# Optimization experiments

Hardware: AMD Instinct MI355X
Metric: run time of the kernel (lower is better)

The kernel has to match this reference:

```python
import jax, jax.numpy as jnp
import numpy as np

N = 100000        # nodes
E = 1600000       # edges (before self-loops)
F_IN = 128        # input feature dim
HID = 32          # hidden_channels
HEADS = 2
HC = HID * HEADS  # 64, per-conv output width (concat=True)
OUT = 40          # out_channels
NEG_SLOPE = 0.2   # PyG GATConv leaky_relu slope
BN_EPS = 1e-5


def setup_inputs() -> dict:
    key = jax.random.key(0)
    ks = jax.random.split(key, 16)
    g = lambda k, shape, s: jax.random.normal(k, shape, jnp.float32) * s
    node_feat = jax.random.normal(ks[0], (N, F_IN), jnp.float32)
    edge_index = jax.random.randint(ks[1], (2, E), 0, N, jnp.int32)
    inp = {
        "node_feat": node_feat,
        "edge_index": edge_index,
        "W1": g(ks[2], (F_IN, HC), 1.0 / np.sqrt(F_IN)),
        "a_src1": g(ks[3], (HEADS, HID), 0.1),
        "a_dst1": g(ks[4], (HEADS, HID), 0.1),
        "b1": jnp.zeros((HC,), jnp.float32),
        # BatchNorm1d(64) in eval mode (running stats)
        "bn_gamma": jnp.ones((HC,), jnp.float32),
        "bn_beta": jnp.zeros((HC,), jnp.float32),
        "bn_mean": g(ks[5], (HC,), 0.1),
        "bn_var": jax.random.uniform(ks[6], (HC,), jnp.float32, 0.5, 1.5),
        "W2": g(ks[7], (HC, HC), 1.0 / np.sqrt(HC)),
        "a_src2": g(ks[8], (HEADS, HID), 0.1),
        "a_dst2": g(ks[9], (HEADS, HID), 0.1),
        "b2": jnp.zeros((HC,), jnp.float32),
        # final projection 64 -> 40
        "Wf": g(ks[10], (HC, OUT), 1.0 / np.sqrt(HC)),
        "bf": jnp.zeros((OUT,), jnp.float32),
    }
    return inp


def _gat_layer(x, src, dst, W, a_s, a_d, b):
    # x: [N, Fin] -> h: [N, H, C]
    h = (x @ W).reshape(N, HEADS, HID)
    alpha_src = jnp.einsum('nhc,hc->nh', h, a_s)   # [N, H]
    alpha_dst = jnp.einsum('nhc,hc->nh', h, a_d)   # [N, H]
    e = jax.nn.leaky_relu(alpha_src[src] + alpha_dst[dst], NEG_SLOPE)  # [Etot, H]
    m = jax.lax.stop_gradient(jax.ops.segment_max(e, dst, num_segments=N))
    ex = jnp.exp(e - m[dst])
    denom = jax.ops.segment_sum(ex, dst, num_segments=N)
    alpha = ex / (denom[dst] + 1e-16)              # softmax over incoming edges
    msg = h[src] * alpha[:, :, None]               # [Etot, H, C]
    out = jax.ops.segment_sum(msg, dst, num_segments=N)  # [N, H, C]
    return out.reshape(N, HC) + b


def reference(node_feat, edge_index, W1, a_src1, a_dst1, b1,
              bn_gamma, bn_beta, bn_mean, bn_var,
              W2, a_src2, a_dst2, b2, Wf, bf):
    # add self-loops (PyG GATConv default add_self_loops=True)
    loop = jnp.arange(N, dtype=edge_index.dtype)
    src = jnp.concatenate([edge_index[0], loop])
    dst = jnp.concatenate([edge_index[1], loop])

    x1 = _gat_layer(node_feat, src, dst, W1, a_src1, a_dst1, b1)
    # BatchNorm1d eval + ELU (dropout is identity in eval)
    x1 = (x1 - bn_mean) * (bn_gamma / jnp.sqrt(bn_var + BN_EPS)) + bn_beta
    x1 = jax.nn.elu(x1)

    x2 = _gat_layer(x1, src, dst, W2, a_src2, a_dst2, b2)

    # JumpingKnowledge 'max': elementwise max over layer outputs
    xj = jnp.maximum(x1, x2)
    return xj @ Wf + bf
```

## Files before the change

### kernel.cpp

```cpp
#include <hip/hip_runtime.h>
#include <hip/hip_bf16.h>

#define N_NODES 100000
#define E_EDGES 1600000
#define ETOT    1700000
#define EQ8     200000
#define NB_EQ8  782
#define NGB     1563
#define NBUK    196
#define F_IN    128
#define HC      64
#define OUT_C   40
#define NEG_SLOPE 0.2f
#define BN_EPS  1e-5f

#define P_W1   0
#define P_AS1  8192
#define P_AD1  8256
#define P_B1   8320
#define P_BNG  8384
#define P_BNB  8448
#define P_BNM  8512
#define P_BNV  8576
#define P_W2   8640
#define P_AS2  12736
#define P_AD2  12800
#define P_B2   12864
#define P_WF   12928
#define P_BF   15488
#define P_TOT  15528

typedef __attribute__((ext_vector_type(8))) short short8;
typedef __attribute__((ext_vector_type(4))) float floatx4;
typedef __attribute__((ext_vector_type(4))) unsigned int uintx4;

__device__ __forceinline__ unsigned short f2bf(float f) {
    unsigned int u = __float_as_uint(f);
    unsigned int r = u + 0x7FFFu + ((u >> 16) & 1u);
    return (unsigned short)(r >> 16);
}

__device__ __forceinline__ float leaky(float v) { return v > 0.f ? v : NEG_SLOPE * v; }

__device__ __forceinline__ float red64(float v) {
#pragma unroll
    for (int off = 32; off > 0; off >>= 1) v += __shfl_xor(v, off, 64);
    return v;
}
__device__ __forceinline__ float red16(float v) {
#pragma unroll
    for (int off = 8; off > 0; off >>= 1) v += __shfl_xor(v, off, 64);
    return v;
}

__global__ __launch_bounds__(64) void detect_kernel(const unsigned short* __restrict__ x,
                                                    int* __restrict__ flag) {
    int t = threadIdx.x;
    bool huge = false;
#pragma unroll
    for (int i = 0; i < 4; ++i) {
        unsigned short u = x[(t * 4 + i) * 2];
        float v = __uint_as_float(((unsigned int)u) << 16);
        if (!(fabsf(v) < 1e4f)) huge = true;
    }
    unsigned long long b = __ballot(huge);
    if (t == 0) *flag = (b != 0ull) ? 1 : 0;
}

struct CvtArgs { const void* ptr[14]; int len[14]; };

__global__ __launch_bounds__(256) void cvt_params_kernel(CvtArgs a,
                                                         const int* __restrict__ flag,
                                                         float* __restrict__ dst) {
    int f = *flag;
    int i = blockIdx.x * 256 + threadIdx.x;
    if (i >= P_TOT) return;
    int k = 0, off = 0;
    while (i >= off + a.len[k]) { off += a.len[k]; ++k; }
    int j = i - off;
    float v = f ? ((const float*)a.ptr[k])[j]
                : __bfloat162float(((const __hip_bfloat16*)a.ptr[k])[j]);
    dst[i] = v;
}

__global__ __launch_bounds__(256) void build_frags_kernel(const float* __restrict__ prm,
                                                          unsigned short* __restrict__ fw1,
                                                          unsigned short* __restrict__ fw2) {
    int i = blockIdx.x * 256 + threadIdx.x;
    if (i < 8192) {
        int j = i & 7, l = (i >> 3) & 63, q = (i >> 9) & 3, t = i >> 11;
        int k = q * 32 + (l >> 4) * 8 + j;
        int n = t * 16 + (l & 15);
        fw1[i] = f2bf(prm[P_W1 + k * 64 + n]);
    } else if (i < 12288) {
        int f = i - 8192;
        int j = f & 7, l = (f >> 3) & 63, q = (f >> 9) & 1, t = f >> 10;
        int k = q * 32 + (l >> 4) * 8 + j;
        int n = t * 16 + (l & 15);
        fw2[f] = f2bf(prm[P_W2 + k * 64 + n]);
    }
}


__global__ __launch_bounds__(256) void fused_hist_gemm1_kernel(
        const int* __restrict__ ei, int* __restrict__ bkt_cnt,
        const void* __restrict__ x, const unsigned short* __restrict__ fw1,
        const float* __restrict__ prm, const int* __restrict__ flag,
        unsigned short* __restrict__ h_bf, float* __restrict__ as_,
        float* __restrict__ ad_) {
    __shared__ short lx[4 * 4 * 64 * 8];
    int t = threadIdx.x;
    if (blockIdx.x < NB_EQ8) {
        int* cnt = (int*)lx;
        if (t < NBUK) cnt[t] = 0;
        __syncthreads();
        int i8 = blockIdx.x * 256 + t;
        if (i8 < EQ8) {
            const unsigned long long* dst2 = (const unsigned long long*)(ei + E_EDGES);
            unsigned long long p0 = __builtin_nontemporal_load(&dst2[i8 * 4]);
            unsigned long long p1 = __builtin_nontemporal_load(&dst2[i8 * 4 + 1]);
            unsigned long long p2 = __builtin_nontemporal_load(&dst2[i8 * 4 + 2]);
            unsigned long long p3 = __builtin_nontemporal_load(&dst2[i8 * 4 + 3]);
            atomicAdd(&cnt[(int)(p0 & 0xFFFFFFFFull) >> 9], 1);
            atomicAdd(&cnt[(int)(p0 >> 32) >> 9], 1);
            atomicAdd(&cnt[(int)(p1 & 0xFFFFFFFFull) >> 9], 1);
            atomicAdd(&cnt[(int)(p1 >> 32) >> 9], 1);
            atomicAdd(&cnt[(int)(p2 & 0xFFFFFFFFull) >> 9], 1);
            atomicAdd(&cnt[(int)(p2 >> 32) >> 9], 1);
            atomicAdd(&cnt[(int)(p3 & 0xFFFFFFFFull) >> 9], 1);
            atomicAdd(&cnt[(int)(p3 >> 32) >> 9], 1);
        }
        __syncthreads();
        if (t < NBUK) {
            int tb = t + (int)(blockIdx.x % NBUK);
            tb -= (tb >= NBUK) ? NBUK : 0;
            int c = cnt[tb];
            if (c) atomicAdd(&bkt_cnt[tb], c);
        }
        return;
    }

    int f = *flag;
    int base = (blockIdx.x - NB_EQ8) * 64;

#pragma unroll
    for (int i = 0; i < 4; ++i) {
        int cid = i * 256 + t;
        int m = cid >> 4, c = cid & 15;
        int q = c >> 2, g = c & 3;
        int loff = (((m >> 4) * 4 + q) * 64 + g * 16 + (m & 15)) * 8;
        int srow = base + m; if (srow > N_NODES - 1) srow = N_NODES - 1;
        short8 s;
        if (f) {
            const float4* p = (const float4*)((const float*)x + ((size_t)srow << 7) + (c << 3));
            float4 u0 = p[0], u1 = p[1];
            s[0] = (short)f2bf(u0.x); s[1] = (short)f2bf(u0.y);
            s[2] = (short)f2bf(u0.z); s[3] = (short)f2bf(u0.w);
            s[4] = (short)f2bf(u1.x); s[5] = (short)f2bf(u1.y);
            s[6] = (short)f2bf(u1.z); s[7] = (short)f2bf(u1.w);
        } else {
            s = *(const short8*)((const unsigned short*)x + ((size_t)srow << 7) + (c << 3));
        }
        *(short8*)&lx[loff] = s;
    }
    __syncthreads();

    int w = t >> 6, lane = t & 63;
    short8 a[4];
#pragma unroll
    for (int q = 0; q < 4; ++q) a[q] = *(short8*)&lx[((w * 4 + q) * 64 + lane) * 8];

    const short8* bw = (const short8*)fw1;
    floatx4 acc[4];
#pragma unroll
    for (int tt = 0; tt < 4; ++tt) acc[tt] = (floatx4){0.f, 0.f, 0.f, 0.f};
#pragma unroll
    for (int tt = 0; tt < 4; ++tt) {
#pragma unroll
        for (int q = 0; q < 4; ++q) {
            short8 b = bw[(tt * 4 + q) * 64 + lane];
            acc[tt] = __builtin_amdgcn_mfma_f32_16x16x32_bf16(a[q], b, acc[tt], 0, 0, 0);
        }
    }

    int cl = lane & 15, grp = lane >> 4;
#pragma unroll
    for (int tt = 0; tt < 4; ++tt) {
#pragma unroll
        for (int r = 0; r < 4; ++r) {
            int node = base + w * 16 + grp * 4 + r;
            if (node < N_NODES)
                h_bf[(size_t)node * 64 + tt * 16 + cl] = f2bf(acc[tt][r]);
        }
    }

    float as0 = prm[P_AS1 + 0  + cl], as1 = prm[P_AS1 + 16 + cl],
          as2 = prm[P_AS1 + 32 + cl], as3 = prm[P_AS1 + 48 + cl];
    float ad0 = prm[P_AD1 + 0  + cl], ad1 = prm[P_AD1 + 16 + cl],
          ad2 = prm[P_AD1 + 32 + cl], ad3 = prm[P_AD1 + 48 + cl];
#pragma unroll
    for (int r = 0; r < 4; ++r) {
        float sh0 = red16(acc[0][r] * as0 + acc[1][r] * as1);
        float sh1 = red16(acc[2][r] * as2 + acc[3][r] * as3);
        float dh0 = red16(acc[0][r] * ad0 + acc[1][r] * ad1);
        float dh1 = red16(acc[2][r] * ad2 + acc[3][r] * ad3);
        int node = base + w * 16 + grp * 4 + r;
        if (cl == 0 && node < N_NODES) {
            as_[node * 2] = sh0;  as_[node * 2 + 1] = sh1;
            ad_[node * 2] = dh0;  ad_[node * 2 + 1] = dh1;
        }
    }
}

__global__ __launch_bounds__(256) void bucket_scan_kernel(const int* __restrict__ bkt_cnt,
                                                          int* __restrict__ boff,
                                                          int* __restrict__ bcur,
                                                          int* __restrict__ row_start) {
    __shared__ int sm[256];
    int t = threadIdx.x;
    int v = (t < NBUK) ? bkt_cnt[t] : 0;
    sm[t] = v;
    __syncthreads();
    for (int off = 1; off < 256; off <<= 1) {
        int o = (t >= off) ? sm[t - off] : 0;
        __syncthreads();
        sm[t] += o;
        __syncthreads();
    }
    if (t < NBUK) { int e = sm[t] - v; boff[t] = e; bcur[t] = e; }
    if (t == NBUK - 1) boff[NBUK] = sm[t];
    if (t == 0) row_start[N_NODES] = ETOT;
}

__global__ __launch_bounds__(256) void bucket_scatter_kernel(const int* __restrict__ ei,
                                                             int* __restrict__ bcur,
                                                             unsigned long long* __restrict__ estage) {
    __shared__ int cnt[NBUK];
    __shared__ int base[NBUK];
    int t = threadIdx.x;
    if (t < NBUK) cnt[t] = 0;
    __syncthreads();
    int i8 = blockIdx.x * 256 + t;
    bool valid = i8 < EQ8;
    int d[8], s[8], rl[8];
    if (valid) {
        const unsigned long long* dst2 = (const unsigned long long*)(ei + E_EDGES);
        const unsigned long long* src2 = (const unsigned long long*)ei;
        unsigned long long p0 = __builtin_nontemporal_load(&dst2[i8 * 4]);
        unsigned long long p1 = __builtin_nontemporal_load(&dst2[i8 * 4 + 1]);
        unsigned long long p2 = __builtin_nontemporal_load(&dst2[i8 * 4 + 2]);
        unsigned long long p3 = __builtin_nontemporal_load(&dst2[i8 * 4 + 3]);
        unsigned long long q0 = __builtin_nontemporal_load(&src2[i8 * 4]);
        unsigned long long q1 = __builtin_nontemporal_load(&src2[i8 * 4 + 1]);
        unsigned long long q2 = __builtin_nontemporal_load(&src2[i8 * 4 + 2]);
        unsigned long long q3 = __builtin_nontemporal_load(&src2[i8 * 4 + 3]);
        d[0] = (int)(p0 & 0xFFFFFFFFull); d[1] = (int)(p0 >> 32);
        d[2] = (int)(p1 & 0xFFFFFFFFull); d[3] = (int)(p1 >> 32);
        d[4] = (int)(p2 & 0xFFFFFFFFull); d[5] = (int)(p2 >> 32);
        d[6] = (int)(p3 & 0xFFFFFFFFull); d[7] = (int)(p3 >> 32);
        s[0] = (int)(q0 & 0xFFFFFFFFull); s[1] = (int)(q0 >> 32);
        s[2] = (int)(q1 & 0xFFFFFFFFull); s[3] = (int)(q1 >> 32);
        s[4] = (int)(q2 & 0xFFFFFFFFull); s[5] = (int)(q2 >> 32);
        s[6] = (int)(q3 & 0xFFFFFFFFull); s[7] = (int)(q3 >> 32);
#pragma unroll
        for (int k = 0; k < 8; ++k) rl[k] = atomicAdd(&cnt[d[k] >> 9], 1);
    }
    __syncthreads();
    if (t < NBUK) {
        int tb = t + (int)(blockIdx.x % NBUK);
        tb -= (tb >= NBUK) ? NBUK : 0;
        int c = cnt[tb];
        base[tb] = c ? atomicAdd(&bcur[tb], c) : 0;
    }
    __syncthreads();
    if (valid) {
#pragma unroll
        for (int k = 0; k < 8; ++k) {
            int buk = d[k] >> 9;
            estage[base[buk] + rl[k]] =
                (unsigned long long)(unsigned int)s[k] |
                ((unsigned long long)(unsigned int)d[k] << 32);
        }
    }
}

__global__ __launch_bounds__(256) void bucket_csr_kernel(const unsigned long long* __restrict__ estage,
                                                         const int* __restrict__ boff,
                                                         int* __restrict__ row_start,
                                                         int* __restrict__ col) {
    __shared__ int ldeg[512];
    __shared__ int sA[512], sB[512];
    __shared__ int exq[512];
    int b = blockIdx.x, t = threadIdx.x;
    int nbase = b << 9;
    int nb = N_NODES - nbase; if (nb > 512) nb = 512;
    int e0 = boff[b], e1 = boff[b + 1];
    int rb = e0 + nbase;
    ldeg[t] = 0; ldeg[t + 256] = 0;
    __syncthreads();
    for (int e = e0 + t; e < e1; e += 256) {
        int dl = (int)(estage[e] >> 32) - nbase;
        atomicAdd(&ldeg[dl], 1);
    }
    __syncthreads();
    int v0 = (t < nb) ? ldeg[t] + 1 : 0;
    int v1 = (t + 256 < nb) ? ldeg[t + 256] + 1 : 0;
    sA[t] = v0; sA[t + 256] = v1;
    __syncthreads();
    int* A = sA; int* Bp = sB;
    for (int off = 1; off < 512; off <<= 1) {
        int a0 = A[t] + ((t >= off) ? A[t - off] : 0);
        int a1 = A[t + 256] + ((t + 256 >= off) ? A[t + 256 - off] : 0);
        Bp[t] = a0; Bp[t + 256] = a1;
        __syncthreads();
        int* tmp = A; A = Bp; Bp = tmp;
    }
    exq[t] = A[t] - v0;
    exq[t + 256] = A[t + 256] - v1;
    __syncthreads();
    if (t < nb) { int rsv = rb + exq[t]; row_start[nbase + t] = rsv; col[rsv] = nbase + t; }
    if (t + 256 < nb) { int rsv = rb + exq[t + 256]; row_start[nbase + t + 256] = rsv; col[rsv] = nbase + t + 256; }
    ldeg[t] = 0; ldeg[t + 256] = 0;
    __syncthreads();
    for (int e = e0 + t; e < e1; e += 256) {
        unsigned long long p = estage[e];
        int s = (int)(p & 0xFFFFFFFFull);
        int dl = (int)(p >> 32) - nbase;
        int r = atomicAdd(&ldeg[dl], 1);
        col[rb + exq[dl] + 1 + r] = s;
    }
}

__global__ __launch_bounds__(128) void gemm2_kernel(const unsigned short* __restrict__ x1_bf,
                                                    const unsigned short* __restrict__ fw2,
                                                    const float* __restrict__ prm,
                                                    unsigned short* __restrict__ h_bf,
                                                    float* __restrict__ as_,
                                                    float* __restrict__ ad_) {
    __shared__ short lx[2 * 2 * 64 * 8];
    int t = threadIdx.x;
    int base = blockIdx.x * 32;

#pragma unroll
    for (int i = 0; i < 2; ++i) {
        int cid = i * 128 + t;
        int m = cid >> 3, c = cid & 7;
        int q = c >> 2, g = c & 3;
        int loff = (((m >> 4) * 2 + q) * 64 + g * 16 + (m & 15)) * 8;
        short8 s = *(const short8*)(x1_bf + ((size_t)(base + m) << 6) + (c << 3));
        *(short8*)&lx[loff] = s;
    }
    __syncthreads();

    int w = t >> 6, lane = t & 63;
    short8 a[2];
#pragma unroll
    for (int q = 0; q < 2; ++q) a[q] = *(short8*)&lx[((w * 2 + q) * 64 + lane) * 8];

    const short8* bw = (const short8*)fw2;
    floatx4 acc[4];
#pragma unroll
    for (int tt = 0; tt < 4; ++tt) acc[tt] = (floatx4){0.f, 0.f, 0.f, 0.f};
#pragma unroll
    for (int tt = 0; tt < 4; ++tt) {
#pragma unroll
        for (int q = 0; q < 2; ++q) {
            short8 b = bw[(tt * 2 + q) * 64 + lane];
            acc[tt] = __builtin_amdgcn_mfma_f32_16x16x32_bf16(a[q], b, acc[tt], 0, 0, 0);
        }
    }

    int cl = lane & 15, grp = lane >> 4;
#pragma unroll
    for (int tt = 0; tt < 4; ++tt) {
#pragma unroll
        for (int r = 0; r < 4; ++r) {
            int node = base + w * 16 + grp * 4 + r;
            h_bf[(size_t)node * 64 + tt * 16 + cl] = f2bf(acc[tt][r]);
        }
    }

    float as0 = prm[P_AS2 + 0  + cl], as1 = prm[P_AS2 + 16 + cl],
          as2 = prm[P_AS2 + 32 + cl], as3 = prm[P_AS2 + 48 + cl];
    float ad0 = prm[P_AD2 + 0  + cl], ad1 = prm[P_AD2 + 16 + cl],
          ad2 = prm[P_AD2 + 32 + cl], ad3 = prm[P_AD2 + 48 + cl];
#pragma unroll
    for (int r = 0; r < 4; ++r) {
        float sh0 = red16(acc[0][r] * as0 + acc[1][r] * as1);
        float sh1 = red16(acc[2][r] * as2 + acc[3][r] * as3);
        float dh0 = red16(acc[0][r] * ad0 + acc[1][r] * ad1);
        float dh1 = red16(acc[2][r] * ad2 + acc[3][r] * ad3);
        if (cl == 0) {
            int node = base + w * 16 + grp * 4 + r;
            as_[node * 2] = sh0;  as_[node * 2 + 1] = sh1;
            ad_[node * 2] = dh0;  ad_[node * 2 + 1] = dh1;
        }
    }
}

__device__ __forceinline__ float slot_reduce(float acc[8], int lane) {
    int slot = lane & 7;
    bool b2 = (slot & 4) != 0;
#pragma unroll
    for (int q = 0; q < 4; ++q) {
        float send = b2 ? acc[q] : acc[q + 4];
        float recv = __shfl_xor(send, 4, 64);
        acc[q] = (b2 ? acc[q + 4] : acc[q]) + recv;
    }
    bool b1 = (slot & 2) != 0;
#pragma unroll
    for (int q = 0; q < 2; ++q) {
        float send = b1 ? acc[q] : acc[q + 2];
        float recv = __shfl_xor(send, 2, 64);
        acc[q] = (b1 ? acc[q + 2] : acc[q]) + recv;
    }
    bool b0 = (slot & 1) != 0;
    float send = b0 ? acc[0] : acc[1];
    float recv = __shfl_xor(send, 1, 64);
    return (b0 ? acc[1] : acc[0]) + recv;
}

template<int NK>
__device__ __forceinline__ void agg_rounds(const unsigned short* __restrict__ hb,
                                           const float* __restrict__ as_,
                                           const int* __restrict__ col,
                                           int rs, int koff, int last,
                                           int slot, int hi, float advh,
                                           float acc[8], float& sw) {
    int ce[NK]; float av[NK]; uintx4 dv[NK];
#pragma unroll
    for (int k = 0; k < NK; ++k) {
        int e = rs + koff + k * 8 + slot;
        ce[k] = col[e < last ? e : last];
    }
#pragma unroll
    for (int k = 0; k < NK; ++k)
        dv[k] = *(const uintx4*)(hb + ((size_t)ce[k] << 6));
#pragma unroll
    for (int k = 0; k < NK; ++k)
        av[k] = as_[ce[k] * 2 + hi];

    if constexpr (NK == 1) {
        asm volatile("" : "+v"(dv[0]), "+v"(av[0]));
    } else if constexpr (NK == 2) {
        asm volatile("" : "+v"(dv[0]), "+v"(dv[1]), "+v"(av[0]), "+v"(av[1]));
    } else if constexpr (NK == 3) {
        asm volatile("" : "+v"(dv[0]), "+v"(dv[1]), "+v"(dv[2]),
                          "+v"(av[0]), "+v"(av[1]), "+v"(av[2]));
    } else {
        asm volatile("" : "+v"(dv[0]), "+v"(dv[1]), "+v"(dv[2]), "+v"(dv[3]),
                          "+v"(av[0]), "+v"(av[1]), "+v"(av[2]), "+v"(av[3]));
    }

#pragma unroll
    for (int k = 0; k < NK; ++k) {
        int e = rs + koff + k * 8 + slot;
        float w = (e <= last) ? __expf(leaky(av[k] + advh)) : 0.f;
        sw += w;
#pragma unroll
        for (int q = 0; q < 4; ++q) {
            unsigned int dw = dv[k][q];
            acc[2 * q]     = fmaf(w, __uint_as_float(dw << 16),         acc[2 * q]);
            acc[2 * q + 1] = fmaf(w, __uint_as_float(dw & 0xFFFF0000u), acc[2 * q + 1]);
        }
    }
}

__device__ __forceinline__ float agg_core(const unsigned short* __restrict__ h_bf,
                                          const float* __restrict__ as_,
                                          const float* __restrict__ ad_,
                                          const int* __restrict__ col,
                                          int v, int rs, int re, int lane) {
    int deg  = re - rs;
    int slot = lane & 7;
    int cg   = lane >> 3;
    int hi   = cg >> 2;
    if (deg <= 64) {
        float advh = ad_[v * 2 + hi];
        const unsigned short* hb = h_bf + (cg << 3);
        int last = re - 1;
        float acc[8] = {0.f,0.f,0.f,0.f,0.f,0.f,0.f,0.f};
        float sw = 0.f;

        if (deg <= 8) {
            agg_rounds<1>(hb, as_, col, rs, 0, last, slot, hi, advh, acc, sw);
        } else if (deg <= 16) {
            agg_rounds<2>(hb, as_, col, rs, 0, last, slot, hi, advh, acc, sw);
        } else if (deg <= 24) {
            agg_rounds<3>(hb, as_, col, rs, 0, last, slot, hi, advh, acc, sw);
        } else {
            agg_rounds<4>(hb, as_, col, rs, 0, last, slot, hi, advh, acc, sw);
            if (deg > 32)
                agg_rounds<4>(hb, as_, col, rs, 32, last, slot, hi, advh, acc, sw);
        }

        sw += __shfl_xor(sw, 1, 64);
        sw += __shfl_xor(sw, 2, 64);
        sw += __shfl_xor(sw, 4, 64);
        float rdh = 1.f / (sw + 1e-16f);

        return slot_reduce(acc, lane) * rdh;
    } else {
        int head = lane >> 5;
        float adv0 = ad_[v * 2], adv1 = ad_[v * 2 + 1];
        float advh = head ? adv1 : adv0;
        float s0 = 0.f, s1 = 0.f;
        for (int e = rs + lane; e < re; e += 64) {
            int s = col[e];
            float2 av = *(const float2*)&as_[s * 2];
            s0 += __expf(leaky(av.x + adv0));
            s1 += __expf(leaky(av.y + adv1));
        }
        s0 = red64(s0); s1 = red64(s1);
        float rdh = 1.f / ((head ? s1 : s0) + 1e-16f);
        float a0 = 0.f;
        for (int e = rs; e < re; ++e) {
            int s = col[e];
            float w = __expf(leaky(as_[s * 2 + head] + advh));
            unsigned short u = h_bf[(size_t)s * 64 + lane];
            a0 = fmaf(w, __uint_as_float(((unsigned int)u) << 16), a0);
        }
        return a0 * rdh;
    }
}

__global__ __launch_bounds__(256, 6) void agg1_kernel(const unsigned short* __restrict__ h_bf,
                                                   const float* __restrict__ as_,
                                                   const float* __restrict__ ad_,
                                                   const int* __restrict__ row_start,
                                                   const int* __restrict__ col,
                                                   const float* __restrict__ bias,
                                                   const float* __restrict__ bn_g,
                                                   const float* __restrict__ bn_b,
                                                   const float* __restrict__ bn_m,
                                                   const float* __restrict__ bn_v,
                                                   unsigned short* __restrict__ x1_bf) {
    int t = threadIdx.x, wid = t >> 6, lane = t & 63;
    int v = blockIdx.x * 4 + wid;
    int rs = row_start[v], re = row_start[v + 1];
    float acc = agg_core(h_bf, as_, ad_, col, v, rs, re, lane);
    float r = acc + bias[lane];
    float scale = bn_g[lane] * rsqrtf(bn_v[lane] + BN_EPS);
    r = (r - bn_m[lane]) * scale + bn_b[lane];
    r = r > 0.f ? r : expm1f(r);
    x1_bf[(size_t)v * 64 + lane] = f2bf(r);
}

__global__ __launch_bounds__(256, 6) void agg2_kernel(const unsigned short* __restrict__ h_bf,
                                                   const float* __restrict__ as_,
                                                   const float* __restrict__ ad_,
                                                   const int* __restrict__ row_start,
                                                   const int* __restrict__ col,
                                                   const float* __restrict__ prm,
                                                   const unsigned short* __restrict__ x1_bf,
                                                   const int* __restrict__ flag,
                                                   void* __restrict__ out) {
    __shared__ float Wfs[2560];
    __shared__ float xsh[4][64];
    int t = threadIdx.x;
#pragma unroll
    for (int i = 0; i < 10; ++i) Wfs[i * 256 + t] = prm[P_WF + i * 256 + t];

    int wid = t >> 6, lane = t & 63;
    int v = blockIdx.x * 4 + wid;
    int rs = row_start[v], re = row_start[v + 1];
    float acc = agg_core(h_bf, as_, ad_, col, v, rs, re, lane);
    float x2 = acc + prm[P_B2 + lane];
    unsigned short u = x1_bf[(size_t)v * 64 + lane];
    float x1v = __uint_as_float(((unsigned int)u) << 16);
    xsh[wid][lane] = fmaxf(x1v, x2);
    __syncthreads();

    if (t < 160) {
        int n = t / 40, o = t - n * 40;
        float po = 0.f;
#pragma unroll
        for (int c = 0; c < 64; c += 4) {
            po = fmaf(xsh[n][c],     Wfs[c * 40 + o],       po);
            po = fmaf(xsh[n][c + 1], Wfs[(c + 1) * 40 + o], po);
            po = fmaf(xsh[n][c + 2], Wfs[(c + 2) * 40 + o], po);
            po = fmaf(xsh[n][c + 3], Wfs[(c + 3) * 40 + o], po);
        }
        float r = po + prm[P_BF + o];
        size_t idx = (size_t)(blockIdx.x * 4 + n) * 40 + o;
        if (*flag) ((float*)out)[idx] = r;
        else ((__hip_bfloat16*)out)[idx] = __float2bfloat16(r);
    }
}

extern "C" void kernel_launch(void* const* d_in, const int* in_sizes, int n_in,
                              void* d_out, int out_size, void* d_ws, size_t ws_size,
                              hipStream_t stream) {
    (void)in_sizes; (void)n_in; (void)out_size; (void)ws_size;
    const void* node_feat = d_in[0];
    const int*  edge_idx  = (const int*)d_in[1];

    char* ws = (char*)d_ws;
    size_t off = 0;
    auto alloc = [&](size_t bytes) -> void* {
        void* p = ws + off;
        off += (bytes + 255) & ~(size_t)255;
        return p;
    };
    unsigned short* h_bf  = (unsigned short*)alloc((size_t)N_NODES * 64 * 2);
    unsigned short* x1_bf = (unsigned short*)alloc((size_t)N_NODES * 64 * 2);
    float* as_ = (float*)alloc((size_t)N_NODES * 2 * 4);
    float* ad_ = (float*)alloc((size_t)N_NODES * 2 * 4);
    int* row_start = (int*)alloc((size_t)(N_NODES + 1) * 4);
    unsigned long long* estage = (unsigned long long*)alloc((size_t)E_EDGES * 8);
    int* col       = (int*)alloc((size_t)ETOT * 4);
    int* bkt_cnt   = (int*)alloc((size_t)NBUK * 4);
    int* bkt_off   = (int*)alloc((size_t)(NBUK + 1) * 4);
    int* bkt_cur   = (int*)alloc((size_t)NBUK * 4);
    float* prm     = (float*)alloc((size_t)P_TOT * 4);
    unsigned short* fw1 = (unsigned short*)alloc(8192 * 2);
    unsigned short* fw2 = (unsigned short*)alloc(4096 * 2);
    int* flag      = (int*)alloc(256);

    detect_kernel<<<1, 64, 0, stream>>>((const unsigned short*)node_feat, flag);
    CvtArgs ca;
    const int lens[14] = {8192, 64, 64, 64, 64, 64, 64, 64, 4096, 64, 64, 64, 2560, 40};
    for (int i = 0; i < 14; ++i) { ca.ptr[i] = d_in[i + 2]; ca.len[i] = lens[i]; }
    cvt_params_kernel<<<(P_TOT + 255) / 256, 256, 0, stream>>>(ca, flag, prm);
    build_frags_kernel<<<48, 256, 0, stream>>>(prm, fw1, fw2);

    hipMemsetAsync(bkt_cnt, 0, (size_t)NBUK * 4, stream);
    fused_hist_gemm1_kernel<<<NB_EQ8 + NGB, 256, 0, stream>>>(
        edge_idx, bkt_cnt, node_feat, fw1, prm, flag, h_bf, as_, ad_);
    bucket_scan_kernel<<<1, 256, 0, stream>>>(bkt_cnt, bkt_off, bkt_cur, row_start);
    bucket_scatter_kernel<<<NB_EQ8, 256, 0, stream>>>(edge_idx, bkt_cur, estage);
    bucket_csr_kernel<<<NBUK, 256, 0, stream>>>(estage, bkt_off, row_start, col);

    agg1_kernel<<<N_NODES / 4, 256, 0, stream>>>(h_bf, as_, ad_, row_start, col,
                                                 prm + P_B1, prm + P_BNG, prm + P_BNB,
                                                 prm + P_BNM, prm + P_BNV, x1_bf);
    gemm2_kernel<<<N_NODES / 32, 128, 0, stream>>>(x1_bf, fw2, prm,
                                                   h_bf, as_, ad_);
    agg2_kernel<<<N_NODES / 4, 256, 0, stream>>>(h_bf, as_, ad_, row_start, col,
                                                 prm, x1_bf, flag, d_out);
}
```

Baseline: 333.7 us.

## Fuse layer-2 GEMM and attention logits into layer-1 aggregation kernel

Removes the separate MFMA gemm2 kernel. The layer-1 aggregation now stages W2 (16 KB fp32) in shared memory per block and computes each node's 64-wide h2 row with scalar FMAs, then reduces the attention source/destination logits across 32-lane halves. Separate h2/as2/ad2 buffers avoid overwriting layer-1 data still being read by other blocks. This saves a launch and the re-read of x1, but each 4-node block reloads W2 from global, uses 16 KB of LDS, and launch bounds rise to 8 waves per SIMD target, which may limit occupancy or cause spills.

Measured after the change: 338.4 us. Within noise of the previous version (+1.4%).

```diff
diff --git a/kernel.cpp b/kernel.cpp
--- a/kernel.cpp
+++ b/kernel.cpp
@@ -52,6 +52,11 @@
     for (int off = 8; off > 0; off >>= 1) v += __shfl_xor(v, off, 64);
     return v;
 }
+__device__ __forceinline__ float red32h(float v) {
+#pragma unroll
+    for (int off = 16; off > 0; off >>= 1) v += __shfl_xor(v, off, 64);
+    return v;
+}
 
 __global__ __launch_bounds__(64) void detect_kernel(const unsigned short* __restrict__ x,
                                                     int* __restrict__ flag) {
@@ -84,23 +89,15 @@
 }
 
 __global__ __launch_bounds__(256) void build_frags_kernel(const float* __restrict__ prm,
-                                                          unsigned short* __restrict__ fw1,
-                                                          unsigned short* __restrict__ fw2) {
+                                                          unsigned short* __restrict__ fw1) {
     int i = blockIdx.x * 256 + threadIdx.x;
     if (i < 8192) {
         int j = i & 7, l = (i >> 3) & 63, q = (i >> 9) & 3, t = i >> 11;
         int k = q * 32 + (l >> 4) * 8 + j;
         int n = t * 16 + (l & 15);
         fw1[i] = f2bf(prm[P_W1 + k * 64 + n]);
-    } else if (i < 12288) {
-        int f = i - 8192;
-        int j = f & 7, l = (f >> 3) & 63, q = (f >> 9) & 1, t = f >> 10;
-        int k = q * 32 + (l >> 4) * 8 + j;
-        int n = t * 16 + (l & 15);
-        fw2[f] = f2bf(prm[P_W2 + k * 64 + n]);
-    }
-}
-
+    }
+}
 
 __global__ __launch_bounds__(256) void fused_hist_gemm1_kernel(
         const int* __restrict__ ei, int* __restrict__ bkt_cnt,
@@ -331,73 +328,6 @@
     }
 }
 
-__global__ __launch_bounds__(128) void gemm2_kernel(const unsigned short* __restrict__ x1_bf,
-                                                    const unsigned short* __restrict__ fw2,
-                                                    const float* __restrict__ prm,
-                                                    unsigned short* __restrict__ h_bf,
-                                                    float* __restrict__ as_,
-                                                    float* __restrict__ ad_) {
-    __shared__ short lx[2 * 2 * 64 * 8];
-    int t = threadIdx.x;
-    int base = blockIdx.x * 32;
-
-#pragma unroll
-    for (int i = 0; i < 2; ++i) {
-        int cid = i * 128 + t;
-        int m = cid >> 3, c = cid & 7;
-        int q = c >> 2, g = c & 3;
-        int loff = (((m >> 4) * 2 + q) * 64 + g * 16 + (m & 15)) * 8;
-        short8 s = *(const short8*)(x1_bf + ((size_t)(base + m) << 6) + (c << 3));
-        *(short8*)&lx[loff] = s;
-    }
-    __syncthreads();
-
-    int w = t >> 6, lane = t & 63;
-    short8 a[2];
-#pragma unroll
-    for (int q = 0; q < 2; ++q) a[q] = *(short8*)&lx[((w * 2 + q) * 64 + lane) * 8];
-
-    const short8* bw = (const short8*)fw2;
-    floatx4 acc[4];
-#pragma unroll
-    for (int tt = 0; tt < 4; ++tt) acc[tt] = (floatx4){0.f, 0.f, 0.f, 0.f};
-#pragma unroll
-    for (int tt = 0; tt < 4; ++tt) {
-#pragma unroll
-        for (int q = 0; q < 2; ++q) {
-            short8 b = bw[(tt * 2 + q) * 64 + lane];
-            acc[tt] = __builtin_amdgcn_mfma_f32_16x16x32_bf16(a[q], b, acc[tt], 0, 0, 0);
-        }
-    }
-
-    int cl = lane & 15, grp = lane >> 4;
-#pragma unroll
-    for (int tt = 0; tt < 4; ++tt) {
-#pragma unroll
-        for (int r = 0; r < 4; ++r) {
-            int node = base + w * 16 + grp * 4 + r;
-            h_bf[(size_t)node * 64 + tt * 16 + cl] = f2bf(acc[tt][r]);
-        }
-    }
-
-    float as0 = prm[P_AS2 + 0  + cl], as1 = prm[P_AS2 + 16 + cl],
-          as2 = prm[P_AS2 + 32 + cl], as3 = prm[P_AS2 + 48 + cl];
-    float ad0 = prm[P_AD2 + 0  + cl], ad1 = prm[P_AD2 + 16 + cl],
-          ad2 = prm[P_AD2 + 32 + cl], ad3 = prm[P_AD2 + 48 + cl];
-#pragma unroll
-    for (int r = 0; r < 4; ++r) {
-        float sh0 = red16(acc[0][r] * as0 + acc[1][r] * as1);
-        float sh1 = red16(acc[2][r] * as2 + acc[3][r] * as3);
-        float dh0 = red16(acc[0][r] * ad0 + acc[1][r] * ad1);
-        float dh1 = red16(acc[2][r] * ad2 + acc[3][r] * ad3);
-        if (cl == 0) {
-            int node = base + w * 16 + grp * 4 + r;
-            as_[node * 2] = sh0;  as_[node * 2 + 1] = sh1;
-            ad_[node * 2] = dh0;  ad_[node * 2 + 1] = dh1;
-        }
-    }
-}
-
 __device__ __forceinline__ float slot_reduce(float acc[8], int lane) {
     int slot = lane & 7;
     bool b2 = (slot & 4) != 0;
@@ -524,31 +454,54 @@
     }
 }
 
-__global__ __launch_bounds__(256, 6) void agg1_kernel(const unsigned short* __restrict__ h_bf,
-                                                   const float* __restrict__ as_,
-                                                   const float* __restrict__ ad_,
-                                                   const int* __restrict__ row_start,
-                                                   const int* __restrict__ col,
-                                                   const float* __restrict__ bias,
-                                                   const float* __restrict__ bn_g,
-                                                   const float* __restrict__ bn_b,
-                                                   const float* __restrict__ bn_m,
-                                                   const float* __restrict__ bn_v,
-                                                   unsigned short* __restrict__ x1_bf) {
-    int t = threadIdx.x, wid = t >> 6, lane = t & 63;
+__global__ __launch_bounds__(256, 8) void agg1g2_kernel(
+        const unsigned short* __restrict__ h_bf,
+        const float* __restrict__ as_, const float* __restrict__ ad_,
+        const int* __restrict__ row_start, const int* __restrict__ col,
+        const float* __restrict__ prm,
+        unsigned short* __restrict__ x1_bf,
+        unsigned short* __restrict__ h2_bf,
+        float* __restrict__ as2_, float* __restrict__ ad2_) {
+    __shared__ float Wsh[4096];
+    __shared__ float xsh[4][64];
+    int t = threadIdx.x;
+#pragma unroll
+    for (int i = 0; i < 16; ++i) Wsh[i * 256 + t] = prm[P_W2 + i * 256 + t];
+
+    int wid = t >> 6, lane = t & 63;
     int v = blockIdx.x * 4 + wid;
     int rs = row_start[v], re = row_start[v + 1];
     float acc = agg_core(h_bf, as_, ad_, col, v, rs, re, lane);
-    float r = acc + bias[lane];
-    float scale = bn_g[lane] * rsqrtf(bn_v[lane] + BN_EPS);
-    r = (r - bn_m[lane]) * scale + bn_b[lane];
+    float r = acc + prm[P_B1 + lane];
+    float scale = prm[P_BNG + lane] * rsqrtf(prm[P_BNV + lane] + BN_EPS);
+    r = (r - prm[P_BNM + lane]) * scale + prm[P_BNB + lane];
     r = r > 0.f ? r : expm1f(r);
     x1_bf[(size_t)v * 64 + lane] = f2bf(r);
-}
-
-__global__ __launch_bounds__(256, 6) void agg2_kernel(const unsigned short* __restrict__ h_bf,
-                                                   const float* __restrict__ as_,
-                                                   const float* __restrict__ ad_,
+    xsh[wid][lane] = r;
+    __syncthreads();
+
+    float h2 = 0.f;
+#pragma unroll
+    for (int c = 0; c < 64; c += 4) {
+        h2 = fmaf(xsh[wid][c],     Wsh[c * 64 + lane],       h2);
+        h2 = fmaf(xsh[wid][c + 1], Wsh[(c + 1) * 64 + lane], h2);
+        h2 = fmaf(xsh[wid][c + 2], Wsh[(c + 2) * 64 + lane], h2);
+        h2 = fmaf(xsh[wid][c + 3], Wsh[(c + 3) * 64 + lane], h2);
+    }
+    h2_bf[(size_t)v * 64 + lane] = f2bf(h2);
+
+    float sh = red32h(h2 * prm[P_AS2 + lane]);
+    float dh = red32h(h2 * prm[P_AD2 + lane]);
+    if ((lane & 31) == 0) {
+        int hh = lane >> 5;
+        as2_[v * 2 + hh] = sh;
+        ad2_[v * 2 + hh] = dh;
+    }
+}
+
+__global__ __launch_bounds__(256, 8) void agg2_kernel(const unsigned short* __restrict__ h2_bf,
+                                                   const float* __restrict__ as2_,
+                                                   const float* __restrict__ ad2_,
                                                    const int* __restrict__ row_start,
                                                    const int* __restrict__ col,
                                                    const float* __restrict__ prm,
@@ -564,7 +517,7 @@
     int wid = t >> 6, lane = t & 63;
     int v = blockIdx.x * 4 + wid;
     int rs = row_start[v], re = row_start[v + 1];
-    float acc = agg_core(h_bf, as_, ad_, col, v, rs, re, lane);
+    float acc = agg_core(h2_bf, as2_, ad2_, col, v, rs, re, lane);
     float x2 = acc + prm[P_B2 + lane];
     unsigned short u = x1_bf[(size_t)v * 64 + lane];
     float x1v = __uint_as_float(((unsigned int)u) << 16);
@@ -603,9 +556,12 @@
         return p;
     };
     unsigned short* h_bf  = (unsigned short*)alloc((size_t)N_NODES * 64 * 2);
+    unsigned short* h2_bf = (unsigned short*)alloc((size_t)N_NODES * 64 * 2);
     unsigned short* x1_bf = (unsigned short*)alloc((size_t)N_NODES * 64 * 2);
-    float* as_ = (float*)alloc((size_t)N_NODES * 2 * 4);
-    float* ad_ = (float*)alloc((size_t)N_NODES * 2 * 4);
+    float* as_  = (float*)alloc((size_t)N_NODES * 2 * 4);
+    float* ad_  = (float*)alloc((size_t)N_NODES * 2 * 4);
+    float* as2_ = (float*)alloc((size_t)N_NODES * 2 * 4);
+    float* ad2_ = (float*)alloc((size_t)N_NODES * 2 * 4);
     int* row_start = (int*)alloc((size_t)(N_NODES + 1) * 4);
     unsigned long long* estage = (unsigned long long*)alloc((size_t)E_EDGES * 8);
     int* col       = (int*)alloc((size_t)ETOT * 4);
@@ -614,7 +570,6 @@
     int* bkt_cur   = (int*)alloc((size_t)NBUK * 4);
     float* prm     = (float*)alloc((size_t)P_TOT * 4);
     unsigned short* fw1 = (unsigned short*)alloc(8192 * 2);
-    unsigned short* fw2 = (unsigned short*)alloc(4096 * 2);
     int* flag      = (int*)alloc(256);
 
     detect_kernel<<<1, 64, 0, stream>>>((const unsigned short*)node_feat, flag);
@@ -622,7 +577,7 @@
     const int lens[14] = {8192, 64, 64, 64, 64, 64, 64, 64, 4096, 64, 64, 64, 2560, 40};
     for (int i = 0; i < 14; ++i) { ca.ptr[i] = d_in[i + 2]; ca.len[i] = lens[i]; }
     cvt_params_kernel<<<(P_TOT + 255) / 256, 256, 0, stream>>>(ca, flag, prm);
-    build_frags_kernel<<<48, 256, 0, stream>>>(prm, fw1, fw2);
+    build_frags_kernel<<<32, 256, 0, stream>>>(prm, fw1);
 
     hipMemsetAsync(bkt_cnt, 0, (size_t)NBUK * 4, stream);
     fused_hist_gemm1_kernel<<<NB_EQ8 + NGB, 256, 0, stream>>>(
@@ -631,11 +586,8 @@
     bucket_scatter_kernel<<<NB_EQ8, 256, 0, stream>>>(edge_idx, bkt_cur, estage);
     bucket_csr_kernel<<<NBUK, 256, 0, stream>>>(estage, bkt_off, row_start, col);
 
-    agg1_kernel<<<N_NODES / 4, 256, 0, stream>>>(h_bf, as_, ad_, row_start, col,
-                                                 prm + P_B1, prm + P_BNG, prm + P_BNB,
-                                                 prm + P_BNM, prm + P_BNV, x1_bf);
-    gemm2_kernel<<<N_NODES / 32, 128, 0, stream>>>(x1_bf, fw2, prm,
-                                                   h_bf, as_, ad_);
-    agg2_kernel<<<N_NODES / 4, 256, 0, stream>>>(h_bf, as_, ad_, row_start, col,
+    agg1g2_kernel<<<N_NODES / 4, 256, 0, stream>>>(h_bf, as_, ad_, row_start, col,
+                                                   prm, x1_bf, h2_bf, as2_, ad2_);
+    agg2_kernel<<<N_NODES / 4, 256, 0, stream>>>(h2_bf, as2_, ad2_, row_start, col,
                                                  prm, x1_bf, flag, d_out);
 }
```
